# Kernel optimization log

Measured on AMD Instinct MI355X. Metric: run time of the kernel, lower is better.

The kernel has to match this reference:

```python
import jax, jax.numpy as jnp
import numpy as np
from jax import lax

H, W = 3072, 4096
BLACK = 0.0625            # black level (normalized)
KNEE_X = np.array([0.0, 0.25, 1.0], np.float32)   # decompanding curve
KNEE_Y = np.array([0.0, 0.50, 1.0], np.float32)
DEN_R, DEN_EPS = 2, 100.0         # BayerDenoise defaults
AWB_MAX_GAIN = 4.0
LTM_A, LTM_B, LTM_R, LTM_EPS = 0.7, 0.0, 8, 1e-3
GAMMA = 2.2


def _box_sum_1d(x, r, axis):
    """Sliding-window sum of width 2r+1 along `axis`, edge-truncated."""
    n = x.shape[axis]
    c = jnp.cumsum(x, axis=axis)
    hi = jnp.clip(jnp.arange(n) + r, 0, n - 1)
    lo = jnp.arange(n) - r - 1
    upper = jnp.take(c, hi, axis=axis)
    lower = jnp.take(c, jnp.clip(lo, 0, n - 1), axis=axis)
    shp = [1] * x.ndim
    shp[axis] = n
    lower = lower * (lo >= 0).astype(x.dtype).reshape(shp)
    return upper - lower


def box_mean(x, r):
    """2D box mean over last two axes, normalized by valid window counts."""
    s = _box_sum_1d(_box_sum_1d(x, r, -2), r, -1)
    cnt = _box_sum_1d(_box_sum_1d(jnp.ones_like(x), r, -2), r, -1)
    return s / cnt


def guided_self(I, r, eps):
    """Self-guided (edge-preserving) filter."""
    m = box_mean(I, r)
    var = box_mean(I * I, r) - m * m
    a = var / (var + eps)
    b = m * (1.0 - a)
    return box_mean(a, r) * I + box_mean(b, r)


def conv3x3(img, k):
    return lax.conv_general_dilated(img[None, None], k[None, None], (1, 1), 'SAME')[0, 0]


def isp_pipeline(x, ccm):
    # --- DecompandBlackLevel: piecewise-linear decompand + black level ---
    x = jnp.interp(x, jnp.asarray(KNEE_X), jnp.asarray(KNEE_Y))
    x = jnp.clip((x - BLACK) / (1.0 - BLACK), 0.0, 1.0)

    # --- BayerDenoise: guided filter on each RGGB plane ---
    p = jnp.stack([x[0::2, 0::2], x[0::2, 1::2], x[1::2, 0::2], x[1::2, 1::2]])  # [4,H/2,W/2]
    p = guided_self(p, DEN_R, DEN_EPS)

    # --- AWB: gray-world gains from plane means (lum mask [0,1] = all pixels) ---
    r_m, g_m, b_m = p[0].mean(), 0.5 * (p[1].mean() + p[2].mean()), p[3].mean()
    gr = jnp.minimum(g_m / (r_m + 1e-8), AWB_MAX_GAIN)
    gb = jnp.minimum(g_m / (b_m + 1e-8), AWB_MAX_GAIN)
    x = (jnp.zeros_like(x)
         .at[0::2, 0::2].set(jnp.clip(p[0] * gr, 0.0, 1.0))
         .at[0::2, 1::2].set(jnp.clip(p[1], 0.0, 1.0))
         .at[1::2, 0::2].set(jnp.clip(p[2], 0.0, 1.0))
         .at[1::2, 1::2].set(jnp.clip(p[3] * gb, 0.0, 1.0)))

    # --- Demosaic: bilinear on RGGB mosaic ---
    ii = (jnp.arange(H) % 2)[:, None]
    jj = (jnp.arange(W) % 2)[None, :]
    mR = ((ii == 0) & (jj == 0)).astype(x.dtype)
    mG = (ii != jj).astype(x.dtype)
    mB = ((ii == 1) & (jj == 1)).astype(x.dtype)
    k_g = jnp.array([[0, 1, 0], [1, 4, 1], [0, 1, 0]], jnp.float32) / 4.0
    k_rb = jnp.array([[1, 2, 1], [2, 4, 2], [1, 2, 1]], jnp.float32) / 4.0
    rgb = jnp.stack([conv3x3(x * mR, k_rb), conv3x3(x * mG, k_g), conv3x3(x * mB, k_rb)])  # [3,H,W]

    # --- CCM ---
    rgb = jnp.clip(jnp.einsum('ij,jhw->ihw', ccm, rgb), 0.0, 1.0)

    wl = jnp.array([0.299, 0.587, 0.114], jnp.float32)
    Y = jnp.einsum('c,chw->hw', wl, rgb)
    Ys = Y.reshape(H // 2, 2, W // 2, 2).mean(axis=(1, 3))
    base = jax.image.resize(guided_self(Ys, LTM_R, LTM_EPS), (H, W), 'bilinear')
    Ynew = LTM_A * base + LTM_B + (Y - base)       # detail_gain=1, threshold=0
    rgb = jnp.clip(rgb * (Ynew / (Y + 1e-6)), 0.0, 1.0)

    # --- Gamma ---
    rgb = jnp.clip(rgb, 1e-6, 1.0) ** (1.0 / GAMMA)
    # hist_norm / post_denoise / saturation / sharpening are identity at defaults

    # --- RGBtoYUV -> NV12 (full range BT.601) ---
    R, G, B = rgb[0], rgb[1], rgb[2]
    Yf = 0.299 * R + 0.587 * G + 0.114 * B
    U = -0.168736 * R - 0.331264 * G + 0.5 * B + 0.5
    V = 0.5 * R - 0.418688 * G - 0.081312 * B + 0.5
    Us = U.reshape(H // 2, 2, W // 2, 2).mean(axis=(1, 3))
    Vs = V.reshape(H // 2, 2, W // 2, 2).mean(axis=(1, 3))
    uv = jnp.stack([Us, Vs], axis=-1).reshape(H // 2, W)  # interleaved UVUV...
    out = jnp.concatenate([Yf.reshape(-1), uv.reshape(-1)]) * 255.0
    return jnp.clip(out, 0.0, 255.0)   # float NV12 codes (pre-quantization)


def setup_inputs() -> dict:
    key = jax.random.key(0)
    k1, k2 = jax.random.split(key)
    x = jax.random.uniform(k1, (H, W), dtype=jnp.float32)
    ccm = jnp.eye(3, dtype=jnp.float32) + 0.1 * jax.random.normal(k2, (3, 3), dtype=jnp.float32)
    return {"x": x, "ccm": ccm}


def reference(x, ccm):
    return isp_pipeline(x, ccm)
```

## Files before the change

### kernel.cpp

```cpp
#include <hip/hip_runtime.h>
#include <math.h>

#define IMG_H 3072
#define IMG_W 4096
#define Hh 1536
#define Wh 2048
#define S (Hh*Wh)

#define TID 32
#define TVL 16
#define HBLK 192

#if __has_builtin(__builtin_amdgcn_rcpf)
#define RCP(x) __builtin_amdgcn_rcpf(x)
#else
#define RCP(x) (1.0f/(x))
#endif

__device__ __forceinline__ float clamp01(float v){ return fminf(fmaxf(v, 0.0f), 1.0f); }

__device__ __forceinline__ float decompand_black(float v){
  float y = (v <= 0.25f) ? (2.0f*v) : fmaf(v - 0.25f, 0.5f/0.75f, 0.5f);
  y = clamp01(y);
  return clamp01((y - 0.0625f) * (1.0f/0.9375f));
}

__device__ __forceinline__ float gamma22(float x){
  return __builtin_amdgcn_exp2f(0.45454545454545453f * __builtin_amdgcn_logf(x));
}

__global__ __launch_bounds__(256) void k_split(const float* __restrict__ x, float* __restrict__ P,
                                               float* __restrict__ sums){
  int idx = blockIdx.x*256 + threadIdx.x;
  int i = idx >> 10, jq = (idx & 1023)*2;
  const float* r0 = x + (size_t)(2*i)*IMG_W + 2*jq;
  float4 a = *(const float4*)r0;
  float4 b = *(const float4*)(r0 + IMG_W);
  size_t o = (size_t)i*Wh + jq;
  *(float2*)(P + o)            = make_float2(decompand_black(a.x), decompand_black(a.z));
  *(float2*)(P + S + o)        = make_float2(decompand_black(a.y), decompand_black(a.w));
  *(float2*)(P + 2*(size_t)S + o) = make_float2(decompand_black(b.x), decompand_black(b.z));
  *(float2*)(P + 3*(size_t)S + o) = make_float2(decompand_black(b.y), decompand_black(b.w));
  if (blockIdx.x == 0 && threadIdx.x < 4) sums[threadIdx.x] = 0.f;
}

template<int TI, bool FAST>
__device__ __forceinline__ void denoise_col2(const float* __restrict__ in, float* __restrict__ D,
                                             int c0, int i0, float& local){
  const float inv25 = 1.0f/25.0f;
  float cw_a[6], amask[6], cw_o0 = 25.f, cw_o1 = 25.f;
  if (!FAST){
    #pragma unroll
    for (int k=0;k<6;++k){
      int pc = c0 + k - 2;
      bool ok = ((unsigned)pc < (unsigned)Wh);
      amask[k] = ok ? 1.f : 0.f;
      cw_a[k]  = ok ? (float)(min(pc+2, Wh-1) - max(pc-2, 0) + 1) : 1.f;
    }
    cw_o0 = (float)(min(c0+2, Wh-1)   - max(c0-2, 0) + 1);
    cw_o1 = (float)(min(c0+3, Wh-1)   - max(c0-1, 0) + 1);
  }

  float rh1[6][5]={{0}}, rh2[6][5]={{0}};
  float vs1[6]={0}, vs2[6]={0};
  float rha0[5]={0}, rhb0[5]={0}, rha1[5]={0}, rhb1[5]={0};
  float cI0[5]={0}, cI1[5]={0};
  float wa0=0.f, wb0=0.f, wa1=0.f, wb1=0.f;

  const float* rp = in + (size_t)(i0-4)*Wh + c0;
  float* wp = D + (size_t)i0*Wh + c0;

  #pragma unroll 5
  for (int rr=0; rr<TI+8; ++rr){
    int r = i0 - 4 + rr;
    float v[10];
    if (FAST){
      float2 p0 = *(const float2*)(rp-4);
      float2 p1 = *(const float2*)(rp-2);
      float2 p2 = *(const float2*)(rp);
      float2 p3 = *(const float2*)(rp+2);
      float2 p4 = *(const float2*)(rp+4);
      v[0]=p0.x; v[1]=p0.y; v[2]=p1.x; v[3]=p1.y; v[4]=p2.x;
      v[5]=p2.y; v[6]=p3.x; v[7]=p3.y; v[8]=p4.x; v[9]=p4.y;
    } else {
      if ((unsigned)r < (unsigned)Hh){
        #pragma unroll
        for (int d=0; d<10; ++d){
          int c = c0 + d - 4;
          v[d] = ((unsigned)c < (unsigned)Wh) ? rp[d-4] : 0.f;
        }
      } else {
        #pragma unroll
        for (int d=0; d<10; ++d) v[d]=0.f;
      }
    }
    rp += Wh;
    float sq[10];
    #pragma unroll
    for (int d=0; d<10; ++d) sq[d]=v[d]*v[d];
    float h1[6], h2[6];
    h1[0]=v[0]+v[1]+v[2]+v[3]+v[4];
    h2[0]=sq[0]+sq[1]+sq[2]+sq[3]+sq[4];
    #pragma unroll
    for (int k=1;k<6;++k){
      h1[k]=h1[k-1]-v[k-1]+v[k+4];
      h2[k]=h2[k-1]-sq[k-1]+sq[k+4];
    }
    #pragma unroll
    for (int k=0;k<6;++k){
      vs1[k]+=h1[k]-rh1[k][0];
      vs2[k]+=h2[k]-rh2[k][0];
      #pragma unroll
      for (int t=0;t<4;++t){ rh1[k][t]=rh1[k][t+1]; rh2[k][t]=rh2[k][t+1]; }
      rh1[k][4]=h1[k]; rh2[k][4]=h2[k];
    }
    #pragma unroll
    for (int t=0;t<4;++t){ cI0[t]=cI0[t+1]; cI1[t]=cI1[t+1]; }
    cI0[4]=v[4]; cI1[4]=v[5];

    if (rr >= 4){
      int q = r-2;
      float a6[6], b6[6];
      if (FAST){
        #pragma unroll
        for (int k=0;k<6;++k){
          float m   = vs1[k]*inv25;
          float var = fmaf(-m, m, vs2[k]*inv25);
          float a   = var*RCP(var + 100.0f);
          a6[k] = a; b6[k] = fmaf(-m, a, m);
        }
      } else {
        float rmask = ((unsigned)q < (unsigned)Hh) ? 1.f : 0.f;
        float rh = (float)(min(q+2, Hh-1) - max(q-2, 0) + 1);
        #pragma unroll
        for (int k=0;k<6;++k){
          float inv = RCP(rh*cw_a[k]);
          float m   = vs1[k]*inv;
          float var = fmaf(-m, m, vs2[k]*inv);
          float a   = var*RCP(var + 100.0f);
          float b   = fmaf(-m, a, m);
          a6[k] = a*amask[k]*rmask; b6[k] = b*amask[k]*rmask;
        }
      }
      float ha0 = a6[0]+a6[1]+a6[2]+a6[3]+a6[4];
      float hb0 = b6[0]+b6[1]+b6[2]+b6[3]+b6[4];
      float ha1 = ha0 - a6[0] + a6[5];
      float hb1 = hb0 - b6[0] + b6[5];
      wa0 += ha0 - rha0[0]; wb0 += hb0 - rhb0[0];
      wa1 += ha1 - rha1[0]; wb1 += hb1 - rhb1[0];
      #pragma unroll
      for (int t=0;t<4;++t){
        rha0[t]=rha0[t+1]; rhb0[t]=rhb0[t+1];
        rha1[t]=rha1[t+1]; rhb1[t]=rhb1[t+1];
      }
      rha0[4]=ha0; rhb0[4]=hb0; rha1[4]=ha1; rhb1[4]=hb1;

      if (rr >= 8){
        int ro = r-4;
        float invo0, invo1;
        if (FAST){ invo0 = inv25; invo1 = inv25; }
        else {
          float rho = (float)(min(ro+2, Hh-1) - max(ro-2, 0) + 1);
          invo0 = RCP(rho*cw_o0); invo1 = RCP(rho*cw_o1);
        }
        float d0 = fmaf(wa0*invo0, cI0[0], wb0*invo0);
        float d1 = fmaf(wa1*invo1, cI1[0], wb1*invo1);
        *(float2*)wp = make_float2(d0, d1); wp += Wh;
        local += d0 + d1;
      }
    }
  }
}

template<int TI>
__global__ __launch_bounds__(256) void k_denoise(const float* __restrict__ P4,
                                                 float* __restrict__ D4,
                                                 float* __restrict__ sums){
  const int c0 = (blockIdx.x*256 + threadIdx.x)*2;
  const int i0 = blockIdx.y*TI;
  const int pl = blockIdx.z;
  const float* __restrict__ in = P4 + (size_t)pl*S;
  float* __restrict__ D = D4 + (size_t)pl*S;
  float local = 0.f;

  const int cmin = (blockIdx.x*256 + (threadIdx.x & ~63))*2;
  const bool rows_ok = (i0 >= 4) && (i0 + TI + 4 <= Hh);
  const bool fast = rows_ok && (cmin >= 4) && (cmin + 131 < Wh);
  if (fast) denoise_col2<TI, true >(in, D, c0, i0, local);
  else      denoise_col2<TI, false>(in, D, c0, i0, local);

  __shared__ float red[256];
  red[threadIdx.x]=local;
  __syncthreads();
  #pragma unroll
  for (int off=128; off>0; off>>=1){
    if (threadIdx.x<off) red[threadIdx.x]+=red[threadIdx.x+off];
    __syncthreads();
  }
  if (threadIdx.x==0) atomicAdd(sums+pl, red[0]);
}

template<bool SQUARE>
__global__ __launch_bounds__(256) void k_ltm_h(const float* __restrict__ X1,
                                               const float* __restrict__ X2,
                                               float* __restrict__ O1,
                                               float* __restrict__ O2){
  const int lane = threadIdx.x & 63;
  const int wave = threadIdx.x >> 6;
  const int row  = blockIdx.y;
  const int ob   = blockIdx.x*HBLK + wave*48;
  const int c    = ob - 8 + lane;
  const size_t rb = (size_t)row*Wh;

  float v1 = 0.f, v2 = 0.f;
  if ((unsigned)c < (unsigned)Wh){
    v1 = X1[rb + c];
    v2 = SQUARE ? v1*v1 : X2[rb + c];
  }
  #pragma unroll
  for (int d=1; d<64; d<<=1){
    float t1 = __shfl_up(v1, d, 64);
    float t2 = __shfl_up(v2, d, 64);
    if (lane >= d){ v1 += t1; v2 += t2; }
  }
  float hi1 = __shfl_down(v1, 16, 64);
  float hi2 = __shfl_down(v2, 16, 64);
  float lo1 = __shfl_up(v1, 1, 64);
  float lo2 = __shfl_up(v2, 1, 64);
  if (lane == 0){ lo1 = 0.f; lo2 = 0.f; }
  int oc = ob + lane;
  if (lane < 48 && oc < Wh){
    O1[rb + oc] = hi1 - lo1;
    O2[rb + oc] = hi2 - lo2;
  }
}

template<int TV>
__global__ __launch_bounds__(256) void k_ltm_vh(const float* __restrict__ H1,
                                                const float* __restrict__ H2,
                                                float* __restrict__ Ha,
                                                float* __restrict__ Hb){
  const int lane = threadIdx.x & 63;
  const int wave = threadIdx.x >> 6;
  const int c    = blockIdx.x*HBLK + wave*48 - 8 + lane;
  const int i0   = blockIdx.y*TV;
  const bool cok = ((unsigned)c < (unsigned)Wh);
  const float cwf = (float)(min(c+8, Wh-1) - max(c-8, 0) + 1);

  float ws1 = 0.f, ws2 = 0.f;
  #pragma unroll
  for (int k=-8; k<=8; ++k){
    int r = i0 + k;
    if (((unsigned)r < (unsigned)Hh) && cok){
      ws1 += H1[(size_t)r*Wh + c];
      ws2 += H2[(size_t)r*Wh + c];
    }
  }
  #pragma unroll
  for (int t=0; t<TV; ++t){
    int i = i0 + t;
    float rhf = (float)(min(i+8, Hh-1) - max(i-8, 0) + 1);
    float inv = 1.0f/(rhf*cwf);
    float m   = ws1*inv;
    float var = fmaf(-m, m, ws2*inv);
    float a   = var/(var + 1e-3f);
    float b   = m*(1.0f - a);
    float pa = a, pb = b;
    #pragma unroll
    for (int d=1; d<64; d<<=1){
      float ta = __shfl_up(pa, d, 64);
      float tb = __shfl_up(pb, d, 64);
      if (lane >= d){ pa += ta; pb += tb; }
    }
    float hia = __shfl_down(pa, 8, 64);
    float hib = __shfl_down(pb, 8, 64);
    float loa = __shfl_up(pa, 9, 64);
    float lob = __shfl_up(pb, 9, 64);
    if (lane < 9){ loa = 0.f; lob = 0.f; }
    if (lane >= 8 && lane < 56 && cok){
      Ha[(size_t)i*Wh + c] = hia - loa;
      Hb[(size_t)i*Wh + c] = hib - lob;
    }
    if (t < TV-1){
      int rn = i+9, ro = i-8;
      float n1=0.f, n2=0.f, o1=0.f, o2=0.f;
      if (cok){
        if (rn < Hh){ n1 = H1[(size_t)rn*Wh + c]; n2 = H2[(size_t)rn*Wh + c]; }
        if (ro >= 0){ o1 = H1[(size_t)ro*Wh + c]; o2 = H2[(size_t)ro*Wh + c]; }
      }
      ws1 += n1 - o1; ws2 += n2 - o2;
    }
  }
}

template<int TV>
__global__ __launch_bounds__(256) void k_ltm_v_fin(const float* __restrict__ Ha,
                                                   const float* __restrict__ Hb,
                                                   const float* __restrict__ Ysrc,
                                                   float* __restrict__ bs){
  const int j  = blockIdx.x*256 + threadIdx.x;
  const int i0 = blockIdx.y*TV;
  const float cwf = (float)(min(j+8, Wh-1) - max(j-8, 0) + 1);
  float wa = 0.f, wb = 0.f;
  #pragma unroll
  for (int k=-8; k<=8; ++k){
    int r = i0 + k;
    if ((unsigned)r < (unsigned)Hh){
      wa += Ha[(size_t)r*Wh + j];
      wb += Hb[(size_t)r*Wh + j];
    }
  }
  #pragma unroll
  for (int t=0; t<TV; ++t){
    int i = i0 + t;
    float rhf = (float)(min(i+8, Hh-1) - max(i-8, 0) + 1);
    float inv = 1.0f/(rhf*cwf);
    bs[(size_t)i*Wh + j] = fmaf(wa*inv, Ysrc[(size_t)i*Wh + j], wb*inv);
    if (t < TV-1){
      int rn = i+9, ro = i-8;
      float na=0.f, nb=0.f, oa=0.f, ob_=0.f;
      if (rn < Hh){ na = Ha[(size_t)rn*Wh + j]; nb = Hb[(size_t)rn*Wh + j]; }
      if (ro >= 0){ oa = Ha[(size_t)ro*Wh + j]; ob_ = Hb[(size_t)ro*Wh + j]; }
      wa += na - oa; wb += nb - ob_;
    }
  }
}

__device__ __forceinline__ void awb_gains(const float* __restrict__ sums, float& gr, float& gb){
  const float invS = 1.0f/(float)S;
  float rm = sums[0]*invS, g1 = sums[1]*invS, g2 = sums[2]*invS, bm = sums[3]*invS;
  float gm = 0.5f*(g1+g2);
  gr = fminf(gm/(rm + 1e-8f), 4.0f);
  gb = fminf(gm/(bm + 1e-8f), 4.0f);
}

__device__ __forceinline__ void load_mosaic2(const float* __restrict__ D, float gr, float gb,
                                             int i, int j, float m[4][6]){
  const float* __restrict__ P0 = D;
  const float* __restrict__ P1 = D + (size_t)S;
  const float* __restrict__ P2 = D + (size_t)2*S;
  const float* __restrict__ P3 = D + (size_t)3*S;
  const bool up = (i > 0), dn = (i < Hh-1), lf = (j > 0), rt = (j+2 < Wh);
  const size_t rc = (size_t)i*Wh + j;
  const size_t ru = rc - Wh, rd = rc + Wh;
  const float2 z = make_float2(0.f, 0.f);
  {
    float2 t3 = up ? *(const float2*)(P3+ru) : z;
    float2 t2 = up ? *(const float2*)(P2+ru) : z;
    m[0][0] = (up&&lf) ? clamp01(P3[ru-1]*gb) : 0.f;
    m[0][1] = clamp01(t2.x);
    m[0][2] = clamp01(t3.x*gb);
    m[0][3] = clamp01(t2.y);
    m[0][4] = clamp01(t3.y*gb);
    m[0][5] = (up&&rt) ? clamp01(P2[ru+2]) : 0.f;
  }
  {
    float2 t1 = *(const float2*)(P1+rc);
    float2 t0 = *(const float2*)(P0+rc);
    m[1][0] = lf ? clamp01(P1[rc-1]) : 0.f;
    m[1][1] = clamp01(t0.x*gr);
    m[1][2] = clamp01(t1.x);
    m[1][3] = clamp01(t0.y*gr);
    m[1][4] = clamp01(t1.y);
    m[1][5] = rt ? clamp01(P0[rc+2]*gr) : 0.f;
  }
  {
    float2 s3 = *(const float2*)(P3+rc);
    float2 s2 = *(const float2*)(P2+rc);
    m[2][0] = lf ? clamp01(P3[rc-1]*gb) : 0.f;
    m[2][1] = clamp01(s2.x);
    m[2][2] = clamp01(s3.x*gb);
    m[2][3] = clamp01(s2.y);
    m[2][4] = clamp01(s3.y*gb);
    m[2][5] = rt ? clamp01(P2[rc+2]) : 0.f;
  }
  {
    float2 u1 = dn ? *(const float2*)(P1+rd) : z;
    float2 u0 = dn ? *(const float2*)(P0+rd) : z;
    m[3][0] = (dn&&lf) ? clamp01(P1[rd-1]) : 0.f;
    m[3][1] = clamp01(u0.x*gr);
    m[3][2] = clamp01(u1.x);
    m[3][3] = clamp01(u0.y*gr);
    m[3][4] = clamp01(u1.y);
    m[3][5] = (dn&&rt) ? clamp01(P0[rd+2]*gr) : 0.f;
  }
}

template<int O>
__device__ __forceinline__ void demosaic_ccm_s(const float m[4][6], const float* __restrict__ C,
                                               float R[2][2], float G[2][2], float Bv[2][2]){
  #define MM(a,b) m[a][(b)+2*O]
  float r[2][2], g[2][2], b[2][2];
  r[0][0] = MM(1,1);
  g[0][0] = 0.25f*(MM(0,1)+MM(2,1)+MM(1,0)+MM(1,2));
  b[0][0] = 0.25f*(MM(0,0)+MM(0,2)+MM(2,0)+MM(2,2));
  r[0][1] = 0.5f*(MM(1,1)+MM(1,3));
  g[0][1] = MM(1,2);
  b[0][1] = 0.5f*(MM(0,2)+MM(2,2));
  r[1][0] = 0.5f*(MM(1,1)+MM(3,1));
  g[1][0] = MM(2,1);
  b[1][0] = 0.5f*(MM(2,0)+MM(2,2));
  r[1][1] = 0.25f*(MM(1,1)+MM(1,3)+MM(3,1)+MM(3,3));
  g[1][1] = 0.25f*(MM(1,2)+MM(3,2)+MM(2,1)+MM(2,3));
  b[1][1] = MM(2,2);
  #undef MM
  #pragma unroll
  for (int a=0; a<2; ++a){
    #pragma unroll
    for (int c=0; c<2; ++c){
      R[a][c]  = clamp01(fmaf(C[2], b[a][c], fmaf(C[1], g[a][c], C[0]*r[a][c])));
      G[a][c]  = clamp01(fmaf(C[5], b[a][c], fmaf(C[4], g[a][c], C[3]*r[a][c])));
      Bv[a][c] = clamp01(fmaf(C[8], b[a][c], fmaf(C[7], g[a][c], C[6]*r[a][c])));
    }
  }
}

__global__ __launch_bounds__(256) void k_ys(const float* __restrict__ D, const float* __restrict__ sums,
                                            const float* __restrict__ C, float* __restrict__ Ys){
  int idx = blockIdx.x*256 + threadIdx.x;
  int i = idx >> 10, j = (idx & 1023)*2;
  float gr, gb; awb_gains(sums, gr, gb);
  float m[4][6]; load_mosaic2(D, gr, gb, i, j, m);
  float y0 = 0.f, y1 = 0.f;
  {
    float R[2][2], G[2][2], Bv[2][2];
    demosaic_ccm_s<0>(m, C, R, G, Bv);
    #pragma unroll
    for (int a=0; a<2; ++a)
      #pragma unroll
      for (int c=0; c<2; ++c)
        y0 += 0.299f*R[a][c] + 0.587f*G[a][c] + 0.114f*Bv[a][c];
  }
  {
    float R[2][2], G[2][2], Bv[2][2];
    demosaic_ccm_s<1>(m, C, R, G, Bv);
    #pragma unroll
    for (int a=0; a<2; ++a)
      #pragma unroll
      for (int c=0; c<2; ++c)
        y1 += 0.299f*R[a][c] + 0.587f*G[a][c] + 0.114f*Bv[a][c];
  }
  *(float2*)(Ys + (size_t)i*Wh + j) = make_float2(0.25f*y0, 0.25f*y1);
}

__global__ __launch_bounds__(256) void k_final(const float* __restrict__ D, const float* __restrict__ sums,
                                               const float* __restrict__ C,
                                               const float* __restrict__ bs, float* __restrict__ out){
  int idx = blockIdx.x*256 + threadIdx.x;
  int i = idx >> 10, j = (idx & 1023)*2;
  float gr, gb; awb_gains(sums, gr, gb);
  float m[4][6]; load_mosaic2(D, gr, gb, i, j, m);

  float bsv[3][4];
  #pragma unroll
  for (int a=0; a<3; ++a){
    int r = min(max(i-1+a, 0), Hh-1);
    const float* br = bs + ((size_t)r<<11);
    bsv[a][0] = br[max(j-1, 0)];
    float2 t = *(const float2*)(br + j);
    bsv[a][1] = t.x; bsv[a][2] = t.y;
    bsv[a][3] = br[min(j+2, Wh-1)];
  }

  float Yrow0[4], Yrow1[4], UV[4];
  #pragma unroll
  for (int o=0; o<2; ++o){
    float R[2][2], G[2][2], Bv[2][2];
    if (o==0) demosaic_ccm_s<0>(m, C, R, G, Bv);
    else      demosaic_ccm_s<1>(m, C, R, G, Bv);
    float base[2][2];
    base[0][0] = 0.0625f*bsv[0][0+o] + 0.1875f*bsv[0][1+o] + 0.1875f*bsv[1][0+o] + 0.5625f*bsv[1][1+o];
    base[0][1] = 0.1875f*bsv[0][1+o] + 0.0625f*bsv[0][2+o] + 0.5625f*bsv[1][1+o] + 0.1875f*bsv[1][2+o];
    base[1][0] = 0.1875f*bsv[1][0+o] + 0.5625f*bsv[1][1+o] + 0.0625f*bsv[2][0+o] + 0.1875f*bsv[2][1+o];
    base[1][1] = 0.5625f*bsv[1][1+o] + 0.1875f*bsv[1][2+o] + 0.1875f*bsv[2][1+o] + 0.0625f*bsv[2][2+o];

    float Uacc = 0.f, Vacc = 0.f;
    #pragma unroll
    for (int a=0; a<2; ++a){
      #pragma unroll
      for (int c=0; c<2; ++c){
        float Yl   = 0.299f*R[a][c] + 0.587f*G[a][c] + 0.114f*Bv[a][c];
        float Ynew = fmaf(0.7f, base[a][c], Yl - base[a][c]);
        float sc   = Ynew/(Yl + 1e-6f);
        float Rg = gamma22(fmaxf(clamp01(R[a][c]*sc),  1e-6f));
        float Gg = gamma22(fmaxf(clamp01(G[a][c]*sc),  1e-6f));
        float Bg = gamma22(fmaxf(clamp01(Bv[a][c]*sc), 1e-6f));
        float Yf = 0.299f*Rg + 0.587f*Gg + 0.114f*Bg;
        float Yq = fminf(fmaxf(Yf*255.0f, 0.0f), 255.0f);
        if (a==0) Yrow0[2*o+c] = Yq; else Yrow1[2*o+c] = Yq;
        Uacc += -0.168736f*Rg - 0.331264f*Gg + 0.5f*Bg + 0.5f;
        Vacc +=  0.5f*Rg - 0.418688f*Gg - 0.081312f*Bg + 0.5f;
      }
    }
    UV[2*o]   = fminf(fmaxf(0.25f*Uacc*255.0f, 0.0f), 255.0f);
    UV[2*o+1] = fminf(fmaxf(0.25f*Vacc*255.0f, 0.0f), 255.0f);
  }
  *(float4*)(out + (size_t)(2*i)*IMG_W   + 2*j) = make_float4(Yrow0[0], Yrow0[1], Yrow0[2], Yrow0[3]);
  *(float4*)(out + (size_t)(2*i+1)*IMG_W + 2*j) = make_float4(Yrow1[0], Yrow1[1], Yrow1[2], Yrow1[3]);
  *(float4*)(out + (size_t)IMG_H*IMG_W + (size_t)i*IMG_W + 2*j) = make_float4(UV[0], UV[1], UV[2], UV[3]);
}

extern "C" void kernel_launch(void* const* d_in, const int* in_sizes, int n_in,
                              void* d_out, int out_size, void* d_ws, size_t ws_size,
                              hipStream_t stream){
  const float* x   = (const float*)d_in[0];
  const float* ccm = (const float*)d_in[1];
  float* ws  = (float*)d_ws;
  float* out = (float*)d_out;

  size_t need = ((size_t)10*S + 8)*sizeof(float);
  if (ws_size < need) return;

  float* P   = ws;
  float* D   = ws + (size_t)4*S;
  float* Ys  = ws + (size_t)8*S;
  float* Hs1 = ws;
  float* Hs2 = ws + (size_t)S;
  float* Ha  = ws + (size_t)2*S;
  float* Hb  = ws + (size_t)3*S;
  float* bs  = ws;
  float* sums = ws + (size_t)10*S;

  const int nb2 = S/512;
  dim3 gdn(Wh/512, Hh/TID, 4);
  dim3 gh((Wh + HBLK - 1)/HBLK, Hh);
  dim3 gvh((Wh + HBLK - 1)/HBLK, Hh/TVL);
  dim3 gv(Wh/256, Hh/TVL);

  k_split<<<nb2, 256, 0, stream>>>(x, P, sums);
  k_denoise<TID><<<gdn, 256, 0, stream>>>(P, D, sums);
  k_ys<<<nb2, 256, 0, stream>>>(D, sums, ccm, Ys);
  k_ltm_h<true ><<<gh, 256, 0, stream>>>(Ys, Ys, Hs1, Hs2);
  k_ltm_vh<TVL><<<gvh, 256, 0, stream>>>(Hs1, Hs2, Ha, Hb);
  k_ltm_v_fin<TVL><<<gv, 256, 0, stream>>>(Ha, Hb, Ys, bs);
  k_final<<<nb2, 256, 0, stream>>>(D, sums, ccm, bs, out);
}
```

Measured before the change: 276.6 us.

## Fuse luminance computation with horizontal LTM box sums in one kernel

Merges the Y-luminance kernel and the horizontal box-sum kernel. Each wave computes Y for a strip of columns with overlapping halos, then does a wave-level prefix scan on per-lane pairs to emit the horizontal sums of Y and Y² directly. This removes one launch and a full re-read of the Y plane. In exchange, the halo columns are recomputed and a more complex shuffle pattern handles pairs of outputs per lane.

```diff
diff --git a/kernel.cpp b/kernel.cpp
--- a/kernel.cpp
+++ b/kernel.cpp
@@ -10,6 +10,7 @@
 #define TID 32
 #define TVL 16
 #define HBLK 192
+#define YSW 110
 
 #if __has_builtin(__builtin_amdgcn_rcpf)
 #define RCP(x) __builtin_amdgcn_rcpf(x)
@@ -200,132 +201,6 @@
   if (threadIdx.x==0) atomicAdd(sums+pl, red[0]);
 }
 
-template<bool SQUARE>
-__global__ __launch_bounds__(256) void k_ltm_h(const float* __restrict__ X1,
-                                               const float* __restrict__ X2,
-                                               float* __restrict__ O1,
-                                               float* __restrict__ O2){
-  const int lane = threadIdx.x & 63;
-  const int wave = threadIdx.x >> 6;
-  const int row  = blockIdx.y;
-  const int ob   = blockIdx.x*HBLK + wave*48;
-  const int c    = ob - 8 + lane;
-  const size_t rb = (size_t)row*Wh;
-
-  float v1 = 0.f, v2 = 0.f;
-  if ((unsigned)c < (unsigned)Wh){
-    v1 = X1[rb + c];
-    v2 = SQUARE ? v1*v1 : X2[rb + c];
-  }
-  #pragma unroll
-  for (int d=1; d<64; d<<=1){
-    float t1 = __shfl_up(v1, d, 64);
-    float t2 = __shfl_up(v2, d, 64);
-    if (lane >= d){ v1 += t1; v2 += t2; }
-  }
-  float hi1 = __shfl_down(v1, 16, 64);
-  float hi2 = __shfl_down(v2, 16, 64);
-  float lo1 = __shfl_up(v1, 1, 64);
-  float lo2 = __shfl_up(v2, 1, 64);
-  if (lane == 0){ lo1 = 0.f; lo2 = 0.f; }
-  int oc = ob + lane;
-  if (lane < 48 && oc < Wh){
-    O1[rb + oc] = hi1 - lo1;
-    O2[rb + oc] = hi2 - lo2;
-  }
-}
-
-template<int TV>
-__global__ __launch_bounds__(256) void k_ltm_vh(const float* __restrict__ H1,
-                                                const float* __restrict__ H2,
-                                                float* __restrict__ Ha,
-                                                float* __restrict__ Hb){
-  const int lane = threadIdx.x & 63;
-  const int wave = threadIdx.x >> 6;
-  const int c    = blockIdx.x*HBLK + wave*48 - 8 + lane;
-  const int i0   = blockIdx.y*TV;
-  const bool cok = ((unsigned)c < (unsigned)Wh);
-  const float cwf = (float)(min(c+8, Wh-1) - max(c-8, 0) + 1);
-
-  float ws1 = 0.f, ws2 = 0.f;
-  #pragma unroll
-  for (int k=-8; k<=8; ++k){
-    int r = i0 + k;
-    if (((unsigned)r < (unsigned)Hh) && cok){
-      ws1 += H1[(size_t)r*Wh + c];
-      ws2 += H2[(size_t)r*Wh + c];
-    }
-  }
-  #pragma unroll
-  for (int t=0; t<TV; ++t){
-    int i = i0 + t;
-    float rhf = (float)(min(i+8, Hh-1) - max(i-8, 0) + 1);
-    float inv = 1.0f/(rhf*cwf);
-    float m   = ws1*inv;
-    float var = fmaf(-m, m, ws2*inv);
-    float a   = var/(var + 1e-3f);
-    float b   = m*(1.0f - a);
-    float pa = a, pb = b;
-    #pragma unroll
-    for (int d=1; d<64; d<<=1){
-      float ta = __shfl_up(pa, d, 64);
-      float tb = __shfl_up(pb, d, 64);
-      if (lane >= d){ pa += ta; pb += tb; }
-    }
-    float hia = __shfl_down(pa, 8, 64);
-    float hib = __shfl_down(pb, 8, 64);
-    float loa = __shfl_up(pa, 9, 64);
-    float lob = __shfl_up(pb, 9, 64);
-    if (lane < 9){ loa = 0.f; lob = 0.f; }
-    if (lane >= 8 && lane < 56 && cok){
-      Ha[(size_t)i*Wh + c] = hia - loa;
-      Hb[(size_t)i*Wh + c] = hib - lob;
-    }
-    if (t < TV-1){
-      int rn = i+9, ro = i-8;
-      float n1=0.f, n2=0.f, o1=0.f, o2=0.f;
-      if (cok){
-        if (rn < Hh){ n1 = H1[(size_t)rn*Wh + c]; n2 = H2[(size_t)rn*Wh + c]; }
-        if (ro >= 0){ o1 = H1[(size_t)ro*Wh + c]; o2 = H2[(size_t)ro*Wh + c]; }
-      }
-      ws1 += n1 - o1; ws2 += n2 - o2;
-    }
-  }
-}
-
-template<int TV>
-__global__ __launch_bounds__(256) void k_ltm_v_fin(const float* __restrict__ Ha,
-                                                   const float* __restrict__ Hb,
-                                                   const float* __restrict__ Ysrc,
-                                                   float* __restrict__ bs){
-  const int j  = blockIdx.x*256 + threadIdx.x;
-  const int i0 = blockIdx.y*TV;
-  const float cwf = (float)(min(j+8, Wh-1) - max(j-8, 0) + 1);
-  float wa = 0.f, wb = 0.f;
-  #pragma unroll
-  for (int k=-8; k<=8; ++k){
-    int r = i0 + k;
-    if ((unsigned)r < (unsigned)Hh){
-      wa += Ha[(size_t)r*Wh + j];
-      wb += Hb[(size_t)r*Wh + j];
-    }
-  }
-  #pragma unroll
-  for (int t=0; t<TV; ++t){
-    int i = i0 + t;
-    float rhf = (float)(min(i+8, Hh-1) - max(i-8, 0) + 1);
-    float inv = 1.0f/(rhf*cwf);
-    bs[(size_t)i*Wh + j] = fmaf(wa*inv, Ysrc[(size_t)i*Wh + j], wb*inv);
-    if (t < TV-1){
-      int rn = i+9, ro = i-8;
-      float na=0.f, nb=0.f, oa=0.f, ob_=0.f;
-      if (rn < Hh){ na = Ha[(size_t)rn*Wh + j]; nb = Hb[(size_t)rn*Wh + j]; }
-      if (ro >= 0){ oa = Ha[(size_t)ro*Wh + j]; ob_ = Hb[(size_t)ro*Wh + j]; }
-      wa += na - oa; wb += nb - ob_;
-    }
-  }
-}
-
 __device__ __forceinline__ void awb_gains(const float* __restrict__ sums, float& gr, float& gb){
   const float invS = 1.0f/(float)S;
   float rm = sums[0]*invS, g1 = sums[1]*invS, g2 = sums[2]*invS, bm = sums[3]*invS;
@@ -415,32 +290,157 @@
   }
 }
 
-__global__ __launch_bounds__(256) void k_ys(const float* __restrict__ D, const float* __restrict__ sums,
-                                            const float* __restrict__ C, float* __restrict__ Ys){
-  int idx = blockIdx.x*256 + threadIdx.x;
-  int i = idx >> 10, j = (idx & 1023)*2;
+__global__ __launch_bounds__(256) void k_ys_h(const float* __restrict__ D, const float* __restrict__ sums,
+                                              const float* __restrict__ C, float* __restrict__ Ys,
+                                              float* __restrict__ H1, float* __restrict__ H2){
+  const int lane = threadIdx.x & 63;
+  const int wave = threadIdx.x >> 6;
+  const int i    = blockIdx.y;
+  const int strip= blockIdx.x*4 + wave;
+  const int base = strip*YSW - 10;
+  const int gc0  = base + 2*lane;
+  const bool cok = ((unsigned)gc0 < (unsigned)Wh);
+
   float gr, gb; awb_gains(sums, gr, gb);
-  float m[4][6]; load_mosaic2(D, gr, gb, i, j, m);
   float y0 = 0.f, y1 = 0.f;
-  {
-    float R[2][2], G[2][2], Bv[2][2];
-    demosaic_ccm_s<0>(m, C, R, G, Bv);
-    #pragma unroll
-    for (int a=0; a<2; ++a)
+  if (cok){
+    float m[4][6]; load_mosaic2(D, gr, gb, i, gc0, m);
+    {
+      float R[2][2], G[2][2], Bv[2][2];
+      demosaic_ccm_s<0>(m, C, R, G, Bv);
       #pragma unroll
-      for (int c=0; c<2; ++c)
-        y0 += 0.299f*R[a][c] + 0.587f*G[a][c] + 0.114f*Bv[a][c];
-  }
-  {
-    float R[2][2], G[2][2], Bv[2][2];
-    demosaic_ccm_s<1>(m, C, R, G, Bv);
-    #pragma unroll
-    for (int a=0; a<2; ++a)
+      for (int a=0; a<2; ++a)
+        #pragma unroll
+        for (int c=0; c<2; ++c)
+          y0 += 0.299f*R[a][c] + 0.587f*G[a][c] + 0.114f*Bv[a][c];
+    }
+    {
+      float R[2][2], G[2][2], Bv[2][2];
+      demosaic_ccm_s<1>(m, C, R, G, Bv);
       #pragma unroll
-      for (int c=0; c<2; ++c)
-        y1 += 0.299f*R[a][c] + 0.587f*G[a][c] + 0.114f*Bv[a][c];
-  }
-  *(float2*)(Ys + (size_t)i*Wh + j) = make_float2(0.25f*y0, 0.25f*y1);
+      for (int a=0; a<2; ++a)
+        #pragma unroll
+        for (int c=0; c<2; ++c)
+          y1 += 0.299f*R[a][c] + 0.587f*G[a][c] + 0.114f*Bv[a][c];
+    }
+    y0 *= 0.25f; y1 *= 0.25f;
+  }
+  const float q1 = y1*y1;
+  float P1 = y0 + y1;
+  float P2 = y0*y0 + q1;
+  #pragma unroll
+  for (int d=1; d<64; d<<=1){
+    float t1 = __shfl_up(P1, d, 64);
+    float t2 = __shfl_up(P2, d, 64);
+    if (lane >= d){ P1 += t1; P2 += t2; }
+  }
+  float Pd4_1 = __shfl_down(P1, 4, 64), Pd4_2 = __shfl_down(P2, 4, 64);
+  float Pu5_1 = __shfl_up(P1, 5, 64),  Pu5_2 = __shfl_up(P2, 5, 64);
+  float Pu4_1 = __shfl_up(P1, 4, 64),  Pu4_2 = __shfl_up(P2, 4, 64);
+  float y1d4  = __shfl_down(y1, 4, 64), y1u4 = __shfl_up(y1, 4, 64);
+  float q1d4  = __shfl_down(q1, 4, 64), q1u4 = __shfl_up(q1, 4, 64);
+
+  if (lane >= 5 && lane < 60 && cok){
+    size_t rb = (size_t)i*Wh + gc0;
+    *(float2*)(Ys + rb) = make_float2(y0, y1);
+    float h1e = (Pd4_1 - y1d4) - Pu5_1;
+    float h2e = (Pd4_2 - q1d4) - Pu5_2;
+    float h1o = Pd4_1 - (Pu4_1 - y1u4);
+    float h2o = Pd4_2 - (Pu4_2 - q1u4);
+    *(float2*)(H1 + rb) = make_float2(h1e, h1o);
+    *(float2*)(H2 + rb) = make_float2(h2e, h2o);
+  }
+}
+
+template<int TV>
+__global__ __launch_bounds__(256) void k_ltm_vh(const float* __restrict__ H1,
+                                                const float* __restrict__ H2,
+                                                float* __restrict__ Ha,
+                                                float* __restrict__ Hb){
+  const int lane = threadIdx.x & 63;
+  const int wave = threadIdx.x >> 6;
+  const int c    = blockIdx.x*HBLK + wave*48 - 8 + lane;
+  const int i0   = blockIdx.y*TV;
+  const bool cok = ((unsigned)c < (unsigned)Wh);
+  const float cwf = (float)(min(c+8, Wh-1) - max(c-8, 0) + 1);
+
+  float ws1 = 0.f, ws2 = 0.f;
+  #pragma unroll
+  for (int k=-8; k<=8; ++k){
+    int r = i0 + k;
+    if (((unsigned)r < (unsigned)Hh) && cok){
+      ws1 += H1[(size_t)r*Wh + c];
+      ws2 += H2[(size_t)r*Wh + c];
+    }
+  }
+  #pragma unroll
+  for (int t=0; t<TV; ++t){
+    int i = i0 + t;
+    float rhf = (float)(min(i+8, Hh-1) - max(i-8, 0) + 1);
+    float inv = 1.0f/(rhf*cwf);
+    float m   = ws1*inv;
+    float var = fmaf(-m, m, ws2*inv);
+    float a   = var/(var + 1e-3f);
+    float b   = m*(1.0f - a);
+    float pa = a, pb = b;
+    #pragma unroll
+    for (int d=1; d<64; d<<=1){
+      float ta = __shfl_up(pa, d, 64);
+      float tb = __shfl_up(pb, d, 64);
+      if (lane >= d){ pa += ta; pb += tb; }
+    }
+    float hia = __shfl_down(pa, 8, 64);
+    float hib = __shfl_down(pb, 8, 64);
+    float loa = __shfl_up(pa, 9, 64);
+    float lob = __shfl_up(pb, 9, 64);
+    if (lane < 9){ loa = 0.f; lob = 0.f; }
+    if (lane >= 8 && lane < 56 && cok){
+      Ha[(size_t)i*Wh + c] = hia - loa;
+      Hb[(size_t)i*Wh + c] = hib - lob;
+    }
+    if (t < TV-1){
+      int rn = i+9, ro = i-8;
+      float n1=0.f, n2=0.f, o1=0.f, o2=0.f;
+      if (cok){
+        if (rn < Hh){ n1 = H1[(size_t)rn*Wh + c]; n2 = H2[(size_t)rn*Wh + c]; }
+        if (ro >= 0){ o1 = H1[(size_t)ro*Wh + c]; o2 = H2[(size_t)ro*Wh + c]; }
+      }
+      ws1 += n1 - o1; ws2 += n2 - o2;
+    }
+  }
+}
+
+template<int TV>
+__global__ __launch_bounds__(256) void k_ltm_v_fin(const float* __restrict__ Ha,
+                                                   const float* __restrict__ Hb,
+                                                   const float* __restrict__ Ysrc,
+                                                   float* __restrict__ bs){
+  const int j  = blockIdx.x*256 + threadIdx.x;
+  const int i0 = blockIdx.y*TV;
+  const float cwf = (float)(min(j+8, Wh-1) - max(j-8, 0) + 1);
+  float wa = 0.f, wb = 0.f;
+  #pragma unroll
+  for (int k=-8; k<=8; ++k){
+    int r = i0 + k;
+    if ((unsigned)r < (unsigned)Hh){
+      wa += Ha[(size_t)r*Wh + j];
+      wb += Hb[(size_t)r*Wh + j];
+    }
+  }
+  #pragma unroll
+  for (int t=0; t<TV; ++t){
+    int i = i0 + t;
+    float rhf = (float)(min(i+8, Hh-1) - max(i-8, 0) + 1);
+    float inv = 1.0f/(rhf*cwf);
+    bs[(size_t)i*Wh + j] = fmaf(wa*inv, Ysrc[(size_t)i*Wh + j], wb*inv);
+    if (t < TV-1){
+      int rn = i+9, ro = i-8;
+      float na=0.f, nb=0.f, oa=0.f, ob_=0.f;
+      if (rn < Hh){ na = Ha[(size_t)rn*Wh + j]; nb = Hb[(size_t)rn*Wh + j]; }
+      if (ro >= 0){ oa = Ha[(size_t)ro*Wh + j]; ob_ = Hb[(size_t)ro*Wh + j]; }
+      wa += na - oa; wb += nb - ob_;
+    }
+  }
 }
 
 __global__ __launch_bounds__(256) void k_final(const float* __restrict__ D, const float* __restrict__ sums,
@@ -523,14 +523,13 @@
 
   const int nb2 = S/512;
   dim3 gdn(Wh/512, Hh/TID, 4);
-  dim3 gh((Wh + HBLK - 1)/HBLK, Hh);
+  dim3 gysh((Wh + 4*YSW - 1)/(4*YSW), Hh);
   dim3 gvh((Wh + HBLK - 1)/HBLK, Hh/TVL);
   dim3 gv(Wh/256, Hh/TVL);
 
   k_split<<<nb2, 256, 0, stream>>>(x, P, sums);
   k_denoise<TID><<<gdn, 256, 0, stream>>>(P, D, sums);
-  k_ys<<<nb2, 256, 0, stream>>>(D, sums, ccm, Ys);
-  k_ltm_h<true ><<<gh, 256, 0, stream>>>(Ys, Ys, Hs1, Hs2);
+  k_ys_h<<<gysh, 256, 0, stream>>>(D, sums, ccm, Ys, Hs1, Hs2);
   k_ltm_vh<TVL><<<gvh, 256, 0, stream>>>(Hs1, Hs2, Ha, Hb);
   k_ltm_v_fin<TVL><<<gv, 256, 0, stream>>>(Ha, Hb, Ys, bs);
   k_final<<<nb2, 256, 0, stream>>>(D, sums, ccm, bs, out);
```

Measured after the change: 268.7 us (median of 2 runs). -2.9%, faster.
